# Optimization experiments

Hardware: AMD Instinct MI355X
Metric: run time of the kernel (lower is better)

## Reference

```python
import jax, jax.numpy as jnp
import numpy as np

B, T, C = 2, 2048, 1024
H = 16
HD = C // H  # 64
BLOCK_SIZE = 2048
ROPE_BASE = 10000.0
NEG_INF = float('-inf')


def setup_inputs() -> dict:
    key = jax.random.key(0)
    k1, k2, k3, k4, k5, k6, k7 = jax.random.split(key, 7)
    x = jax.random.normal(k1, (B, T, C), dtype=jnp.float32)
    cumulative_scores = jax.random.normal(k2, (B, T), dtype=jnp.float32)
    padding_mask = jnp.ones((B, BLOCK_SIZE), dtype=jnp.bool_)
    token_index = jax.random.randint(k3, (B, T), 0, BLOCK_SIZE, dtype=jnp.int32)
    c_attn_weight = 0.02 * jax.random.normal(k4, (C, 3 * C), dtype=jnp.float32)
    c_attn_bias = jnp.zeros((3 * C,), dtype=jnp.float32)
    c_proj_weight = 0.02 * jax.random.normal(k5, (C, C), dtype=jnp.float32)
    c_proj_bias = jnp.zeros((C,), dtype=jnp.float32)
    return {
        'x': x,
        'cumulative_scores': cumulative_scores,
        'padding_mask': padding_mask,
        'token_index': token_index,
        'c_attn_weight': c_attn_weight,
        'c_attn_bias': c_attn_bias,
        'c_proj_weight': c_proj_weight,
        'c_proj_bias': c_proj_bias,
    }


def _rotate_half(x):
    x1, x2 = x[..., : x.shape[-1] // 2], x[..., x.shape[-1] // 2:]
    return jnp.concatenate((-x2, x1), axis=-1)


def _forward(x, cumulative_scores, c_attn_weight, c_attn_bias, c_proj_weight,
             c_proj_bias, token_index, padding_mask):
    # qkv projection
    qkv = x @ c_attn_weight + c_attn_bias
    q, k, v = jnp.split(qkv, 3, axis=2)
    q = q.reshape(B, T, H, HD).transpose(0, 2, 1, 3)  # [B,H,T,HD]
    k = k.reshape(B, T, H, HD).transpose(0, 2, 1, 3)
    v = v.reshape(B, T, H, HD).transpose(0, 2, 1, 3)

    # data-dependent per-token rotation amounts (faithful to source: the
    # scatter x.at[..., idx].add(1) with 2D idx accumulates over all batches)
    token_counts = jnp.zeros((B, BLOCK_SIZE), dtype=token_index.dtype)
    token_counts = token_counts.at[..., token_index].add(1)
    inv_counts = 1.0 / (token_counts + 1e-10)  # [B, BLOCK_SIZE] float32
    partial_rotations = jnp.cumsum(
        jnp.take_along_axis(inv_counts, token_index, axis=-1), axis=-1)  # [B,T]

    # RoPE with per-token t
    inv_freq = 1.0 / ROPE_BASE ** (jnp.arange(0, HD, 2, dtype=jnp.float32) / HD)
    freqs = jnp.einsum('bt,j->btj', partial_rotations, inv_freq)  # [B,T,HD/2]
    emb = jnp.concatenate((freqs, freqs), axis=-1)  # [B,T,HD]
    cos = jnp.cos(emb)[:, None, :, :]  # [B,1,T,HD]
    sin = jnp.sin(emb)[:, None, :, :]
    q = q * cos + _rotate_half(q) * sin
    k = k * cos + _rotate_half(k) * sin

    # fork plan: overwrite last channel of q with ones, of k with cum scores
    q = q.at[:, :, :, -1].set(1.0)
    k = k.at[:, :, :, -1].set(jnp.broadcast_to(cumulative_scores[:, None, :], (B, H, T)))

    # causal + padding additive mask
    causal = jnp.where(jnp.tril(jnp.ones((T, T), dtype=jnp.bool_)), 0.0, NEG_INF)  # [T,T]
    pm = jnp.take_along_axis(padding_mask, token_index, axis=1).astype(jnp.float32)  # [B,T]
    pm_outer = pm[:, :, None] * pm[:, None, :]  # [B,T,T]
    pm_add = jnp.where(pm_outer.astype(jnp.bool_), 0.0, NEG_INF)
    mask = causal[None, :, :] + pm_add  # [B,T,T]

    # v scaled by exp(cumulative_scores) along L
    v = v * jnp.exp(cumulative_scores)[:, None, :, None]

    scale = 1.0 / jnp.sqrt(jnp.asarray(HD, dtype=jnp.float32))
    attn = jnp.einsum('bnqd,bnkd->bnqk', q, k) * scale + mask[:, None, :, :]
    attn = jax.nn.softmax(attn, axis=-1)
    y = jnp.einsum('bnqk,bnkd->bnqd', attn, v)
    y = y.transpose(0, 2, 1, 3).reshape(B, T, C)
    return y @ c_proj_weight + c_proj_bias


def reference(x, cumulative_scores, padding_mask, token_index, c_attn_weight,
              c_attn_bias, c_proj_weight, c_proj_bias):
    return _forward(x, cumulative_scores, c_attn_weight, c_attn_bias,
                    c_proj_weight, c_proj_bias, token_index, padding_mask)
```

## Files before the change

kernel.cpp:

```cpp
#include <hip/hip_runtime.h>
#include <hip/hip_bf16.h>
#include <math.h>

#define Bb 2
#define Tt 2048
#define Cc 1024
#define Hh 16
#define HDd 64
#define QSCALE 0.18033688011112042f

typedef __attribute__((ext_vector_type(8))) short short8;
typedef __attribute__((ext_vector_type(4))) short short4v;
typedef __attribute__((ext_vector_type(4))) float f32x4;

#if defined(__has_builtin)
#if __has_builtin(__builtin_amdgcn_global_load_lds)
#define USE_GLL 1
#endif
#endif
#define AS_GLOBAL __attribute__((address_space(1)))
#define AS_LDS    __attribute__((address_space(3)))

__device__ __forceinline__ float bf2f(unsigned short u){
  union { unsigned int i; float f; } v; v.i = ((unsigned int)u)<<16; return v.f;
}
__device__ __forceinline__ unsigned short f2bf(float f){
  union { float f; unsigned int i; } v; v.f = f;
  unsigned int x = v.i;
  return (unsigned short)((x + 0x7fffu + ((x>>16)&1u)) >> 16);
}
__device__ __forceinline__ unsigned int cvtpk_bf16(float lo, float hi){
  unsigned int r;
  asm("v_cvt_pk_bf16_f32 %0, %1, %2" : "=v"(r) : "v"(lo), "v"(hi));
  return r;
}
__device__ __forceinline__ float exp2fast(float x){
  float r; asm("v_exp_f32 %0, %1" : "=v"(r) : "v"(x)); return r;
}
__device__ __forceinline__ f32x4 mfma16(short4v a, short4v b, f32x4 c){
#if defined(__has_builtin)
#if __has_builtin(__builtin_amdgcn_mfma_f32_16x16x16_bf16)
  return __builtin_amdgcn_mfma_f32_16x16x16_bf16(a, b, c, 0, 0, 0);
#elif __has_builtin(__builtin_amdgcn_mfma_f32_16x16x16bf16_1k)
  return __builtin_amdgcn_mfma_f32_16x16x16bf16_1k(a, b, c, 0, 0, 0);
#else
  asm("v_mfma_f32_16x16x16_bf16 %0, %1, %2, %3" : "=v"(c) : "v"(a), "v"(b), "0"(c));
  return c;
#endif
#else
  asm("v_mfma_f32_16x16x16_bf16 %0, %1, %2, %3" : "=v"(c) : "v"(a), "v"(b), "0"(c));
  return c;
#endif
}

__global__ __launch_bounds__(256) void k_f2b(const float* __restrict__ in,
                                             unsigned short* __restrict__ out, int n){
  int i = (blockIdx.x*256 + threadIdx.x)*8;
  if (i >= n) return;
  float4 v0 = *(const float4*)(in + i);
  float4 v1 = *(const float4*)(in + i + 4);
  union { unsigned int u[4]; int4 v; } pk;
  pk.u[0] = cvtpk_bf16(v0.x, v0.y);
  pk.u[1] = cvtpk_bf16(v0.z, v0.w);
  pk.u[2] = cvtpk_bf16(v1.x, v1.y);
  pk.u[3] = cvtpk_bf16(v1.z, v1.w);
  *(int4*)(out + i) = pk.v;
}

__global__ __launch_bounds__(256) void k_transpose_f2b(const float* __restrict__ in,
                                                       unsigned short* __restrict__ out,
                                                       int K, int N){
  __shared__ float tile[32][33];
  int kb = blockIdx.y*32, nb = blockIdx.x*32;
  int tx = threadIdx.x, ty = threadIdx.y;
  #pragma unroll
  for (int i=0;i<4;i++)
    tile[ty+i*8][tx] = in[(size_t)(kb+ty+i*8)*N + nb + tx];
  __syncthreads();
  #pragma unroll
  for (int i=0;i<4;i++)
    out[(size_t)(nb+ty+i*8)*K + kb + tx] = f2bf(tile[tx][ty+i*8]);
}

__global__ __launch_bounds__(1024) void k_scan(const int* __restrict__ tok,
                                               float* __restrict__ cs_t){
  __shared__ int cnt[2048];
  __shared__ float vals[2048];
  __shared__ float psum[1024];
  int b = blockIdx.x;
  int tid = threadIdx.x;
  cnt[tid] = 0; cnt[tid+1024] = 0;
  __syncthreads();
  for (int i = tid; i < Bb*Tt; i += 1024) atomicAdd(&cnt[tok[i]], 1);
  __syncthreads();
  for (int i = tid; i < Tt; i += 1024){
    int idx = tok[b*Tt + i];
    vals[i] = 1.0f / ((float)cnt[idx] + 1e-10f);
  }
  __syncthreads();
  float s0 = vals[2*tid], s1 = vals[2*tid+1];
  psum[tid] = s0 + s1;
  __syncthreads();
  for (int off=1; off<1024; off<<=1){
    float add = (tid>=off) ? psum[tid-off] : 0.0f;
    __syncthreads();
    psum[tid] += add;
    __syncthreads();
  }
  float base = (tid>0) ? psum[tid-1] : 0.0f;
  vals[2*tid]   = base + s0;
  vals[2*tid+1] = base + s0 + s1;
  __syncthreads();
  for (int i = tid; i < Tt*32; i += 1024){
    int t = i >> 5, j = i & 31;
    float invf = exp2f(-(float)j * 0.4152410118609203f);
    float ang = vals[t] * invf;
    float2 cs = make_float2(cosf(ang), sinf(ang));
    *(float2*)&cs_t[((size_t)b*Tt + t)*64 + 2*j] = cs;
  }
}

__global__ __launch_bounds__(256, 4) void k_gemmQKV(const unsigned short* __restrict__ A,
                                                    const unsigned short* __restrict__ Bt,
                                                    const float* __restrict__ bias,
                                                    const float* __restrict__ cs_t,
                                                    const float* __restrict__ cum,
                                                    unsigned short* __restrict__ Qo,
                                                    unsigned short* __restrict__ Ko,
                                                    unsigned short* __restrict__ VTo){
  __shared__ union {
    unsigned short ab[2][128][32];
    unsigned short vb[32][140];
  } sm;
  const int K = 1024, N = 3072;
  int mb = blockIdx.y*128, nb = blockIdx.x*128;
  int tid = threadIdx.x;
  int wave = tid>>6, lane = tid&63;
  int wr = wave>>1, wc = wave&1;
  int lrow = lane&15, lhi = lane>>4;
  f32x4 acc[4][4] = {};
  int r0 = tid>>2;
  int gd = tid&3;
  int gs0 = (gd ^ ((r0>>1)&3)) << 3;
  const unsigned short* Arow0 = A  + (size_t)(mb + r0)*K      + gs0;
  const unsigned short* Arow1 = A  + (size_t)(mb + r0 + 64)*K + gs0;
  const unsigned short* Brow0 = Bt + (size_t)(nb + r0)*K      + gs0;
  const unsigned short* Brow1 = Bt + (size_t)(nb + r0 + 64)*K + gs0;
#ifdef USE_GLL
  for (int kb=0; kb<K; kb+=32){
    __builtin_amdgcn_global_load_lds((const AS_GLOBAL void*)(Arow0 + kb),
                                     (AS_LDS void*)&sm.ab[0][r0][gd*8],    16, 0, 0);
    __builtin_amdgcn_global_load_lds((const AS_GLOBAL void*)(Arow1 + kb),
                                     (AS_LDS void*)&sm.ab[0][r0+64][gd*8], 16, 0, 0);
    __builtin_amdgcn_global_load_lds((const AS_GLOBAL void*)(Brow0 + kb),
                                     (AS_LDS void*)&sm.ab[1][r0][gd*8],    16, 0, 0);
    __builtin_amdgcn_global_load_lds((const AS_GLOBAL void*)(Brow1 + kb),
                                     (AS_LDS void*)&sm.ab[1][r0+64][gd*8], 16, 0, 0);
    __syncthreads();
    short8 af[4], bf[4];
    #pragma unroll
    for (int m=0;m<4;m++){
      int R = 64*wr + 16*m + lrow;
      af[m] = *(const short8*)&sm.ab[0][R][(lhi^((R>>1)&3))<<3];
    }
    #pragma unroll
    for (int n=0;n<4;n++){
      int R = 64*wc + 16*n + lrow;
      bf[n] = *(const short8*)&sm.ab[1][R][(lhi^((R>>1)&3))<<3];
    }
    #pragma unroll
    for (int m=0;m<4;m++)
      #pragma unroll
      for (int n=0;n<4;n++)
        acc[m][n] = __builtin_amdgcn_mfma_f32_16x16x32_bf16(af[m], bf[n], acc[m][n], 0,0,0);
    __syncthreads();
  }
#else
  for (int kb=0; kb<K; kb+=32){
    int4 a0 = *(const int4*)(Arow0 + kb);
    int4 a1 = *(const int4*)(Arow1 + kb);
    int4 b0 = *(const int4*)(Brow0 + kb);
    int4 b1 = *(const int4*)(Brow1 + kb);
    __syncthreads();
    *(int4*)&sm.ab[0][r0][gd*8]    = a0;
    *(int4*)&sm.ab[0][r0+64][gd*8] = a1;
    *(int4*)&sm.ab[1][r0][gd*8]    = b0;
    *(int4*)&sm.ab[1][r0+64][gd*8] = b1;
    __syncthreads();
    short8 af[4], bf[4];
    #pragma unroll
    for (int m=0;m<4;m++){
      int R = 64*wr + 16*m + lrow;
      af[m] = *(const short8*)&sm.ab[0][R][(lhi^((R>>1)&3))<<3];
    }
    #pragma unroll
    for (int n=0;n<4;n++){
      int R = 64*wc + 16*n + lrow;
      bf[n] = *(const short8*)&sm.ab[1][R][(lhi^((R>>1)&3))<<3];
    }
    #pragma unroll
    for (int m=0;m<4;m++)
      #pragma unroll
      for (int n=0;n<4;n++)
        acc[m][n] = __builtin_amdgcn_mfma_f32_16x16x32_bf16(af[m], bf[n], acc[m][n], 0,0,0);
  }
#endif
  int type = nb >> 10;
  int h0 = (nb >> 6) & 15;
  int h  = h0 + wc;
  int b_ = mb >> 11;
  int tb_ = mb & 2047;
  float bz[4];
  #pragma unroll
  for (int n=0;n<4;n++) bz[n] = bias[nb + 64*wc + 16*n + lrow];

  if (type < 2){
    unsigned short* dst = (type==0) ? Qo : Ko;
    #pragma unroll
    for (int m=0;m<4;m++)
      #pragma unroll
      for (int q=0;q<4;q++){
        int rl = 64*wr + 16*m + 4*lhi + q;
        int row = mb + rl;
        float2 cs0 = *(const float2*)&cs_t[(size_t)row*64 + 2*lrow];
        float2 cs1 = *(const float2*)&cs_t[(size_t)row*64 + 32 + 2*lrow];
        float a0 = acc[m][0][q] + bz[0];
        float a1 = acc[m][1][q] + bz[1];
        float a2 = acc[m][2][q] + bz[2];
        float a3 = acc[m][3][q] + bz[3];
        float r0v = a0*cs0.x - a2*cs0.y;
        float r1v = a1*cs1.x - a3*cs1.y;
        float r2v = a2*cs0.x + a0*cs0.y;
        float r3v = a3*cs1.x + a1*cs1.y;
        if (type==0){
          if (lrow==15) r3v = 1.0f;
          r0v *= QSCALE; r1v *= QSCALE; r2v *= QSCALE; r3v *= QSCALE;
        } else {
          if (lrow==15) r3v = cum[row];
        }
        size_t base = (((size_t)b_*Hh + h)*Tt + (row & 2047))*HDd + lrow;
        dst[base]      = f2bf(r0v);
        dst[base + 16] = f2bf(r1v);
        dst[base + 32] = f2bf(r2v);
        dst[base + 48] = f2bf(r3v);
      }
  } else {
    for (int pass=0; pass<4; pass++){
      __syncthreads();
      if (wr == (pass>>1)){
        int m0 = 2*(pass&1);
        #pragma unroll
        for (int mm=0; mm<2; mm++){
          int m = m0 + mm;
          #pragma unroll
          for (int q=0;q<4;q++){
            int rl32 = 16*mm + 4*lhi + q;
            float vs = __expf(cum[mb + 32*pass + rl32]);
            sm.vb[rl32][64*wc + lrow]      = f2bf((acc[m][0][q]+bz[0])*vs);
            sm.vb[rl32][64*wc + 16+lrow]   = f2bf((acc[m][1][q]+bz[1])*vs);
            sm.vb[rl32][64*wc + 32+lrow]   = f2bf((acc[m][2][q]+bz[2])*vs);
            sm.vb[rl32][64*wc + 48+lrow]   = f2bf((acc[m][3][q]+bz[3])*vs);
          }
        }
      }
      __syncthreads();
      #pragma unroll
      for (int i=0;i<16;i++){
        int idx = i*256 + tid;
        int t_l = idx & 31;
        int dh  = idx >> 5;
        int d   = dh & 63;
        int hh  = dh >> 6;
        VTo[(((size_t)b_*Hh + h0 + hh)*HDd + d)*Tt + tb_ + 32*pass + t_l] = sm.vb[t_l][64*hh + d];
      }
    }
  }
}

__global__ __launch_bounds__(256) void k_gemm64(const unsigned short* __restrict__ A,
                                                const unsigned short* __restrict__ Bt,
                                                const float* __restrict__ bias,
                                                float* __restrict__ Cout,
                                                int M, int N, int K){
  __shared__ unsigned short As[64][32];
  __shared__ unsigned short Bs[128][32];
  int mb = blockIdx.y*64, nb = blockIdx.x*128;
  int tid = threadIdx.x;
  int wave = tid>>6, lane = tid&63;
  int wr = wave>>1, wc = wave&1;
  int lrow = lane&15, lhi = lane>>4;
  f32x4 acc[2][4] = {};
  int r0 = tid>>2;
  int gd = tid&3;
  int gs0 = (gd ^ ((r0>>1)&3)) << 3;
  const unsigned short* Arow  = A  + (size_t)(mb + r0)*K      + gs0;
  const unsigned short* Brow0 = Bt + (size_t)(nb + r0)*K      + gs0;
  const unsigned short* Brow1 = Bt + (size_t)(nb + r0 + 64)*K + gs0;
#ifdef USE_GLL
  for (int kb=0; kb<K; kb+=32){
    __builtin_amdgcn_global_load_lds((const AS_GLOBAL void*)(Arow + kb),
                                     (AS_LDS void*)&As[r0][gd*8],    16, 0, 0);
    __builtin_amdgcn_global_load_lds((const AS_GLOBAL void*)(Brow0 + kb),
                                     (AS_LDS void*)&Bs[r0][gd*8],    16, 0, 0);
    __builtin_amdgcn_global_load_lds((const AS_GLOBAL void*)(Brow1 + kb),
                                     (AS_LDS void*)&Bs[r0+64][gd*8], 16, 0, 0);
    __syncthreads();
    short8 af[2], bf[4];
    #pragma unroll
    for (int m=0;m<2;m++){
      int R = 32*wr + 16*m + lrow;
      af[m] = *(const short8*)&As[R][(lhi^((R>>1)&3))<<3];
    }
    #pragma unroll
    for (int n=0;n<4;n++){
      int R = 64*wc + 16*n + lrow;
      bf[n] = *(const short8*)&Bs[R][(lhi^((R>>1)&3))<<3];
    }
    #pragma unroll
    for (int m=0;m<2;m++)
      #pragma unroll
      for (int n=0;n<4;n++)
        acc[m][n] = __builtin_amdgcn_mfma_f32_16x16x32_bf16(af[m], bf[n], acc[m][n], 0,0,0);
    __syncthreads();
  }
#else
  for (int kb=0; kb<K; kb+=32){
    int4 a0 = *(const int4*)(Arow + kb);
    int4 b0 = *(const int4*)(Brow0 + kb);
    int4 b1 = *(const int4*)(Brow1 + kb);
    __syncthreads();
    *(int4*)&As[r0][gd*8]    = a0;
    *(int4*)&Bs[r0][gd*8]    = b0;
    *(int4*)&Bs[r0+64][gd*8] = b1;
    __syncthreads();
    short8 af[2], bf[4];
    #pragma unroll
    for (int m=0;m<2;m++){
      int R = 32*wr + 16*m + lrow;
      af[m] = *(const short8*)&As[R][(lhi^((R>>1)&3))<<3];
    }
    #pragma unroll
    for (int n=0;n<4;n++){
      int R = 64*wc + 16*n + lrow;
      bf[n] = *(const short8*)&Bs[R][(lhi^((R>>1)&3))<<3];
    }
    #pragma unroll
    for (int m=0;m<2;m++)
      #pragma unroll
      for (int n=0;n<4;n++)
        acc[m][n] = __builtin_amdgcn_mfma_f32_16x16x32_bf16(af[m], bf[n], acc[m][n], 0,0,0);
  }
#endif
  #pragma unroll
  for (int m=0;m<2;m++)
    #pragma unroll
    for (int n=0;n<4;n++)
      #pragma unroll
      for (int q=0;q<4;q++){
        int row = mb + 32*wr + 16*m + 4*lhi + q;
        int col = nb + 64*wc + 16*n + lrow;
        Cout[(size_t)row*N + col] = acc[m][n][q] + bias[col];
      }
}

__global__ __launch_bounds__(512, 4) void k_attn8(const unsigned short* __restrict__ Q,
                                                  const unsigned short* __restrict__ K,
                                                  const unsigned short* __restrict__ VT,
                                                  unsigned short* __restrict__ Y){
  __shared__ __align__(16) char smem[65536];
  typedef unsigned short (*tile_t)[2][4096];
  tile_t Ks = (tile_t)smem;
  tile_t Vs = (tile_t)(smem + 32768);
  float (*cmb)[64][35] = (float (*)[64][35])smem;

  int bh = blockIdx.y; int b = bh >> 4, h = bh & 15;
  int s_ = blockIdx.x;
  int tid = threadIdx.x;
  int wave = tid>>6, lane = tid&63;
  int wpair = wave & 3, p = wave >> 2;
  int lrow = lane&15, lhi = lane>>4;
  const unsigned short* Qh = Q + (((size_t)b*Hh + h)*Tt)*HDd;
  const unsigned short* Kh = K + (((size_t)b*Hh + h)*Tt)*HDd;
  const unsigned short* Vh = VT + (((size_t)b*Hh + h)*HDd)*Tt;
  int qL0 = 64*s_ + 16*wpair;
  int qH0 = 1984 - 64*s_ + 16*wpair;
  short8 qfL0 = *(const short8*)&Qh[(size_t)(qL0+lrow)*HDd + 8*lhi];
  short8 qfL1 = *(const short8*)&Qh[(size_t)(qL0+lrow)*HDd + 32 + 8*lhi];
  short8 qfH0 = *(const short8*)&Qh[(size_t)(qH0+lrow)*HDd + 8*lhi];
  short8 qfH1 = *(const short8*)&Qh[(size_t)(qH0+lrow)*HDd + 32 + 8*lhi];
  f32x4 oL[4] = {}, oH[4] = {};
  float lsL = 0.0f, lsH = 0.0f;
  int rowL = qL0 + lrow, rowH = qH0 + lrow;
  int ntL = s_ + 1;
  int NTH = 32 - s_;
  int NI  = (NTH + 1) >> 1;

  int kr = tid >> 3, kc = tid & 7;
  int o_ = tid * 16;
  int ksrc = kr*HDd + ((kc ^ (kr&7)) << 3);
  int vsrc = kr*Tt  + ((kc ^ (kr&7)) << 3);

#ifdef USE_GLL
#define STAGE2(bufi, base_) do { \
    __builtin_amdgcn_global_load_lds((const AS_GLOBAL void*)(Kh + (size_t)(base_)*64*HDd + ksrc), \
        (AS_LDS void*)((AS_LDS char*)&Ks[bufi][0][0] + o_), 16, 0, 0); \
    __builtin_amdgcn_global_load_lds((const AS_GLOBAL void*)(Vh + (size_t)(base_)*64 + vsrc), \
        (AS_LDS void*)((AS_LDS char*)&Vs[bufi][0][0] + o_), 16, 0, 0); \
    if ((base_)+1 < NTH){ \
      __builtin_amdgcn_global_load_lds((const AS_GLOBAL void*)(Kh + (size_t)((base_)+1)*64*HDd + ksrc), \
          (AS_LDS void*)((AS_LDS char*)&Ks[bufi][1][0] + o_), 16, 0, 0); \
      __builtin_amdgcn_global_load_lds((const AS_GLOBAL void*)(Vh + (size_t)((base_)+1)*64 + vsrc), \
          (AS_LDS void*)((AS_LDS char*)&Vs[bufi][1][0] + o_), 16, 0, 0); \
    } \
  } while(0)
#else
#define STAGE2(bufi, base_) do { \
    int4 a_ = *(const int4*)(Kh + (size_t)(base_)*64*HDd + ksrc); \
    int4 c_ = *(const int4*)(Vh + (size_t)(base_)*64 + vsrc); \
    *(int4*)((char*)&Ks[bufi][0][0] + o_) = a_; \
    *(int4*)((char*)&Vs[bufi][0][0] + o_) = c_; \
    if ((base_)+1 < NTH){ \
      int4 b_ = *(const int4*)(Kh + (size_t)((base_)+1)*64*HDd + ksrc); \
      int4 d_ = *(const int4*)(Vh + (size_t)((base_)+1)*64 + vsrc); \
      *(int4*)((char*)&Ks[bufi][1][0] + o_) = b_; \
      *(int4*)((char*)&Vs[bufi][1][0] + o_) = d_; \
    } \
  } while(0)
#endif

  STAGE2(0, 0);
  int buf = 0;
  for (int i = 0; i < NI; i++){
    __syncthreads();
    if (i+1 < NI) STAGE2(buf^1, 2*(i+1));
    int kt = 2*i + p;
    if (kt < NTH){
      int k0 = kt*64;
      bool doL = (kt < ntL);
      const unsigned short* Kbase = &Ks[buf][p][0];
      const unsigned short* Vbase = &Vs[buf][p][0];
      f32x4 sL[4] = {}, sH[4] = {};
      __builtin_amdgcn_s_setprio(1);
      #pragma unroll
      for (int j=0;j<4;j++){
        int krow = 16*j + lrow;
        #pragma unroll
        for (int ks=0;ks<2;ks++){
          int dgrp = (4*ks + lhi) ^ (krow&7);
          short8 kf = *(const short8*)&Kbase[krow*64 + dgrp*8];
          sH[j] = __builtin_amdgcn_mfma_f32_16x16x32_bf16(kf, ks ? qfH1 : qfH0, sH[j], 0,0,0);
          if (doL) sL[j] = __builtin_amdgcn_mfma_f32_16x16x32_bf16(kf, ks ? qfL1 : qfL0, sL[j], 0,0,0);
        }
      }
      __builtin_amdgcn_s_setprio(0);
      short4v paH[4], paL[4];
      {
        bool diagH = (k0 + 63 >= qH0);
        #pragma unroll
        for (int j=0;j<4;j++){
          int kbase = k0 + 16*j + 4*lhi;
          float p0 = exp2fast(sH[j][0]);
          float p1 = exp2fast(sH[j][1]);
          float p2 = exp2fast(sH[j][2]);
          float p3 = exp2fast(sH[j][3]);
          if (diagH){
            if (kbase + 0 > rowH) p0 = 0.0f;
            if (kbase + 1 > rowH) p1 = 0.0f;
            if (kbase + 2 > rowH) p2 = 0.0f;
            if (kbase + 3 > rowH) p3 = 0.0f;
          }
          lsH += (p0 + p1) + (p2 + p3);
          union { unsigned int u[2]; short4v v; } pk;
          pk.u[0] = cvtpk_bf16(p0, p1);
          pk.u[1] = cvtpk_bf16(p2, p3);
          paH[j] = pk.v;
        }
      }
      if (doL){
        bool diagL = (k0 + 63 >= qL0);
        #pragma unroll
        for (int j=0;j<4;j++){
          int kbase = k0 + 16*j + 4*lhi;
          float p0 = exp2fast(sL[j][0]);
          float p1 = exp2fast(sL[j][1]);
          float p2 = exp2fast(sL[j][2]);
          float p3 = exp2fast(sL[j][3]);
          if (diagL){
            if (kbase + 0 > rowL) p0 = 0.0f;
            if (kbase + 1 > rowL) p1 = 0.0f;
            if (kbase + 2 > rowL) p2 = 0.0f;
            if (kbase + 3 > rowL) p3 = 0.0f;
          }
          lsL += (p0 + p1) + (p2 + p3);
          union { unsigned int u[2]; short4v v; } pk;
          pk.u[0] = cvtpk_bf16(p0, p1);
          pk.u[1] = cvtpk_bf16(p2, p3);
          paL[j] = pk.v;
        }
      }
      __builtin_amdgcn_s_setprio(1);
      #pragma unroll
      for (int jp=0;jp<4;jp++){
        int vrow = 16*jp + lrow;
        #pragma unroll
        for (int j=0;j<4;j++){
          int byte_in_row = ((((2*j + (lhi>>1)) ^ (vrow&7)) << 4) | ((lhi&1) << 3));
          short4v vf = *(const short4v*)((const char*)&Vbase[vrow*64] + byte_in_row);
          oH[jp] = mfma16(vf, paH[j], oH[jp]);
          if (doL) oL[jp] = mfma16(vf, paL[j], oL[jp]);
        }
      }
      __builtin_amdgcn_s_setprio(0);
    }
    buf ^= 1;
  }

  __syncthreads();
  if (p == 1){
    float* c = &cmb[wpair][lane][0];
    #pragma unroll
    for (int jp=0;jp<4;jp++)
      #pragma unroll
      for (int r=0;r<4;r++){
        c[4*jp+r]    = oL[jp][r];
        c[16+4*jp+r] = oH[jp][r];
      }
    c[32] = lsL; c[33] = lsH;
  }
  __syncthreads();
  if (p == 0){
    const float* c = &cmb[wpair][lane][0];
    #pragma unroll
    for (int jp=0;jp<4;jp++)
      #pragma unroll
      for (int r=0;r<4;r++){
        oL[jp][r] += c[4*jp+r];
        oH[jp][r] += c[16+4*jp+r];
      }
    lsL += c[32]; lsH += c[33];
    lsL += __shfl_xor(lsL, 16); lsL += __shfl_xor(lsL, 32);
    lsH += __shfl_xor(lsH, 16); lsH += __shfl_xor(lsH, 32);
    float invL = 1.0f / lsL, invH = 1.0f / lsH;
    size_t rbL = ((size_t)b*Tt + qL0 + lrow)*Cc + h*HDd + 4*lhi;
    size_t rbH = ((size_t)b*Tt + qH0 + lrow)*Cc + h*HDd + 4*lhi;
    #pragma unroll
    for (int jp=0;jp<4;jp++){
      unsigned int l0 = cvtpk_bf16(oL[jp][0]*invL, oL[jp][1]*invL);
      unsigned int l1 = cvtpk_bf16(oL[jp][2]*invL, oL[jp][3]*invL);
      unsigned int h0_ = cvtpk_bf16(oH[jp][0]*invH, oH[jp][1]*invH);
      unsigned int h1_ = cvtpk_bf16(oH[jp][2]*invH, oH[jp][3]*invH);
      *(unsigned long long*)&Y[rbL + 16*jp] = (unsigned long long)l0 | ((unsigned long long)l1<<32);
      *(unsigned long long*)&Y[rbH + 16*jp] = (unsigned long long)h0_ | ((unsigned long long)h1_<<32);
    }
  }
#undef STAGE2
}

extern "C" void kernel_launch(void* const* d_in, const int* in_sizes, int n_in,
                              void* d_out, int out_size, void* d_ws, size_t ws_size,
                              hipStream_t stream){
  const float* x     = (const float*)d_in[0];
  const float* cum   = (const float*)d_in[1];
  const int*   tok   = (const int*)d_in[3];
  const float* Wqkv  = (const float*)d_in[4];
  const float* bqkv  = (const float*)d_in[5];
  const float* Wproj = (const float*)d_in[6];
  const float* bproj = (const float*)d_in[7];

  char* ws = (char*)d_ws;
  size_t off = 0;
  auto alloc = [&](size_t bytes)->void*{
    void* p = ws + off; off += (bytes + 255) & ~(size_t)255; return p;
  };
  unsigned short* wqkvT = (unsigned short*)alloc((size_t)3072*1024*2);
  unsigned short* wprojT= (unsigned short*)alloc((size_t)1024*1024*2);
  unsigned short* xb    = (unsigned short*)alloc((size_t)4096*1024*2);
  unsigned short* Qb    = (unsigned short*)alloc((size_t)Bb*Hh*Tt*HDd*2);
  unsigned short* Kb    = (unsigned short*)alloc((size_t)Bb*Hh*Tt*HDd*2);
  unsigned short* VTb   = (unsigned short*)alloc((size_t)Bb*Hh*Tt*HDd*2);
  float* cs_t           = (float*)alloc((size_t)Bb*Tt*64*4);
  unsigned short* Y     = xb;

  k_f2b<<<dim3(4096*1024/8/256), dim3(256), 0, stream>>>(x, xb, 4096*1024);
  k_transpose_f2b<<<dim3(3072/32, 1024/32), dim3(32,8), 0, stream>>>(Wqkv, wqkvT, 1024, 3072);
  k_transpose_f2b<<<dim3(1024/32, 1024/32), dim3(32,8), 0, stream>>>(Wproj, wprojT, 1024, 1024);
  k_scan<<<dim3(Bb), dim3(1024), 0, stream>>>(tok, cs_t);
  k_gemmQKV<<<dim3(3072/128, 4096/128), dim3(256), 0, stream>>>(xb, wqkvT, bqkv, cs_t, cum, Qb, Kb, VTb);
  k_attn8<<<dim3(16, Bb*Hh), dim3(512), 0, stream>>>(Qb, Kb, VTb, Y);
  k_gemm64<<<dim3(1024/128, 4096/64), dim3(256), 0, stream>>>(Y, wprojT, bproj, (float*)d_out, 4096, 1024, 1024);
}
```

Measured before the change: 140.2 us.

## Widen QKV GEMM K-step to 64 and single-buffer attention LDS for occupancy

The QKV GEMM now stages a 64-wide K slice per iteration with an 8-way XOR swizzle. That halves the number of barrier pairs and issues two MFMA sub-steps per load. The attention kernel drops its double-buffered K/V LDS tiles in favour of a single buffer (36 KB instead of 64 KB) and raises launch bounds to 8 blocks per SM to get more resident waves. The cost is that loads are no longer prefetched behind compute in attention, and an extra barrier is added per iteration.

```diff
diff --git a/kernel.cpp b/kernel.cpp
--- a/kernel.cpp
+++ b/kernel.cpp
@@ -129,7 +129,7 @@
                                                     unsigned short* __restrict__ Ko,
                                                     unsigned short* __restrict__ VTo){
   __shared__ union {
-    unsigned short ab[2][128][32];
+    unsigned short ab[2][128][64];
     unsigned short vb[32][140];
   } sm;
   const int K = 1024, N = 3072;
@@ -139,70 +139,78 @@
   int wr = wave>>1, wc = wave&1;
   int lrow = lane&15, lhi = lane>>4;
   f32x4 acc[4][4] = {};
-  int r0 = tid>>2;
-  int gd = tid&3;
-  int gs0 = (gd ^ ((r0>>1)&3)) << 3;
-  const unsigned short* Arow0 = A  + (size_t)(mb + r0)*K      + gs0;
-  const unsigned short* Arow1 = A  + (size_t)(mb + r0 + 64)*K + gs0;
-  const unsigned short* Brow0 = Bt + (size_t)(nb + r0)*K      + gs0;
-  const unsigned short* Brow1 = Bt + (size_t)(nb + r0 + 64)*K + gs0;
+  int r0 = tid>>3;
+  int g0 = tid&7;
+  int gsw = (g0 ^ (r0&7)) << 3;
+  const unsigned short* Asrc = A  + (size_t)(mb + r0)*K + gsw;
+  const unsigned short* Bsrc = Bt + (size_t)(nb + r0)*K + gsw;
+  const size_t rstep = (size_t)32*K;
 #ifdef USE_GLL
-  for (int kb=0; kb<K; kb+=32){
-    __builtin_amdgcn_global_load_lds((const AS_GLOBAL void*)(Arow0 + kb),
-                                     (AS_LDS void*)&sm.ab[0][r0][gd*8],    16, 0, 0);
-    __builtin_amdgcn_global_load_lds((const AS_GLOBAL void*)(Arow1 + kb),
-                                     (AS_LDS void*)&sm.ab[0][r0+64][gd*8], 16, 0, 0);
-    __builtin_amdgcn_global_load_lds((const AS_GLOBAL void*)(Brow0 + kb),
-                                     (AS_LDS void*)&sm.ab[1][r0][gd*8],    16, 0, 0);
-    __builtin_amdgcn_global_load_lds((const AS_GLOBAL void*)(Brow1 + kb),
-                                     (AS_LDS void*)&sm.ab[1][r0+64][gd*8], 16, 0, 0);
-    __syncthreads();
-    short8 af[4], bf[4];
-    #pragma unroll
-    for (int m=0;m<4;m++){
-      int R = 64*wr + 16*m + lrow;
-      af[m] = *(const short8*)&sm.ab[0][R][(lhi^((R>>1)&3))<<3];
-    }
-    #pragma unroll
-    for (int n=0;n<4;n++){
-      int R = 64*wc + 16*n + lrow;
-      bf[n] = *(const short8*)&sm.ab[1][R][(lhi^((R>>1)&3))<<3];
-    }
-    #pragma unroll
-    for (int m=0;m<4;m++)
-      #pragma unroll
-      for (int n=0;n<4;n++)
-        acc[m][n] = __builtin_amdgcn_mfma_f32_16x16x32_bf16(af[m], bf[n], acc[m][n], 0,0,0);
+  for (int kb=0; kb<K; kb+=64){
+    #pragma unroll
+    for (int i=0;i<4;i++){
+      __builtin_amdgcn_global_load_lds((const AS_GLOBAL void*)(Asrc + i*rstep + kb),
+                                       (AS_LDS void*)&sm.ab[0][r0+32*i][g0*8], 16, 0, 0);
+      __builtin_amdgcn_global_load_lds((const AS_GLOBAL void*)(Bsrc + i*rstep + kb),
+                                       (AS_LDS void*)&sm.ab[1][r0+32*i][g0*8], 16, 0, 0);
+    }
+    __syncthreads();
+    #pragma unroll
+    for (int ks=0; ks<2; ks++){
+      short8 af[4], bf[4];
+      #pragma unroll
+      for (int m=0;m<4;m++){
+        int R = 64*wr + 16*m + lrow;
+        af[m] = *(const short8*)&sm.ab[0][R][((4*ks+lhi)^(R&7))<<3];
+      }
+      #pragma unroll
+      for (int n=0;n<4;n++){
+        int R = 64*wc + 16*n + lrow;
+        bf[n] = *(const short8*)&sm.ab[1][R][((4*ks+lhi)^(R&7))<<3];
+      }
+      #pragma unroll
+      for (int m=0;m<4;m++)
+        #pragma unroll
+        for (int n=0;n<4;n++)
+          acc[m][n] = __builtin_amdgcn_mfma_f32_16x16x32_bf16(af[m], bf[n], acc[m][n], 0,0,0);
+    }
     __syncthreads();
   }
 #else
-  for (int kb=0; kb<K; kb+=32){
-    int4 a0 = *(const int4*)(Arow0 + kb);
-    int4 a1 = *(const int4*)(Arow1 + kb);
-    int4 b0 = *(const int4*)(Brow0 + kb);
-    int4 b1 = *(const int4*)(Brow1 + kb);
-    __syncthreads();
-    *(int4*)&sm.ab[0][r0][gd*8]    = a0;
-    *(int4*)&sm.ab[0][r0+64][gd*8] = a1;
-    *(int4*)&sm.ab[1][r0][gd*8]    = b0;
-    *(int4*)&sm.ab[1][r0+64][gd*8] = b1;
-    __syncthreads();
-    short8 af[4], bf[4];
-    #pragma unroll
-    for (int m=0;m<4;m++){
-      int R = 64*wr + 16*m + lrow;
-      af[m] = *(const short8*)&sm.ab[0][R][(lhi^((R>>1)&3))<<3];
-    }
-    #pragma unroll
-    for (int n=0;n<4;n++){
-      int R = 64*wc + 16*n + lrow;
-      bf[n] = *(const short8*)&sm.ab[1][R][(lhi^((R>>1)&3))<<3];
-    }
-    #pragma unroll
-    for (int m=0;m<4;m++)
-      #pragma unroll
-      for (int n=0;n<4;n++)
-        acc[m][n] = __builtin_amdgcn_mfma_f32_16x16x32_bf16(af[m], bf[n], acc[m][n], 0,0,0);
+  for (int kb=0; kb<K; kb+=64){
+    int4 st[8];
+    #pragma unroll
+    for (int i=0;i<4;i++){
+      st[2*i]   = *(const int4*)(Asrc + i*rstep + kb);
+      st[2*i+1] = *(const int4*)(Bsrc + i*rstep + kb);
+    }
+    __syncthreads();
+    #pragma unroll
+    for (int i=0;i<4;i++){
+      *(int4*)&sm.ab[0][r0+32*i][g0*8] = st[2*i];
+      *(int4*)&sm.ab[1][r0+32*i][g0*8] = st[2*i+1];
+    }
+    __syncthreads();
+    #pragma unroll
+    for (int ks=0; ks<2; ks++){
+      short8 af[4], bf[4];
+      #pragma unroll
+      for (int m=0;m<4;m++){
+        int R = 64*wr + 16*m + lrow;
+        af[m] = *(const short8*)&sm.ab[0][R][((4*ks+lhi)^(R&7))<<3];
+      }
+      #pragma unroll
+      for (int n=0;n<4;n++){
+        int R = 64*wc + 16*n + lrow;
+        bf[n] = *(const short8*)&sm.ab[1][R][((4*ks+lhi)^(R&7))<<3];
+      }
+      #pragma unroll
+      for (int m=0;m<4;m++)
+        #pragma unroll
+        for (int n=0;n<4;n++)
+          acc[m][n] = __builtin_amdgcn_mfma_f32_16x16x32_bf16(af[m], bf[n], acc[m][n], 0,0,0);
+    }
+    __syncthreads();
   }
 #endif
   int type = nb >> 10;
@@ -363,14 +371,13 @@
       }
 }
 
-__global__ __launch_bounds__(512, 4) void k_attn8(const unsigned short* __restrict__ Q,
-                                                  const unsigned short* __restrict__ K,
-                                                  const unsigned short* __restrict__ VT,
-                                                  unsigned short* __restrict__ Y){
-  __shared__ __align__(16) char smem[65536];
-  typedef unsigned short (*tile_t)[2][4096];
-  tile_t Ks = (tile_t)smem;
-  tile_t Vs = (tile_t)(smem + 32768);
+__global__ __launch_bounds__(512, 8) void k_attn10(const unsigned short* __restrict__ Q,
+                                                   const unsigned short* __restrict__ K,
+                                                   const unsigned short* __restrict__ VT,
+                                                   unsigned short* __restrict__ Y){
+  __shared__ __align__(16) char smem[36864];
+  unsigned short (*Ks)[4096] = (unsigned short (*)[4096])smem;
+  unsigned short (*Vs)[4096] = (unsigned short (*)[4096])(smem + 16384);
   float (*cmb)[64][35] = (float (*)[64][35])smem;
 
   int bh = blockIdx.y; int b = bh >> 4, h = bh & 15;
@@ -401,44 +408,43 @@
   int vsrc = kr*Tt  + ((kc ^ (kr&7)) << 3);
 
 #ifdef USE_GLL
-#define STAGE2(bufi, base_) do { \
+#define STAGE2(base_) do { \
     __builtin_amdgcn_global_load_lds((const AS_GLOBAL void*)(Kh + (size_t)(base_)*64*HDd + ksrc), \
-        (AS_LDS void*)((AS_LDS char*)&Ks[bufi][0][0] + o_), 16, 0, 0); \
+        (AS_LDS void*)((AS_LDS char*)&Ks[0][0] + o_), 16, 0, 0); \
     __builtin_amdgcn_global_load_lds((const AS_GLOBAL void*)(Vh + (size_t)(base_)*64 + vsrc), \
-        (AS_LDS void*)((AS_LDS char*)&Vs[bufi][0][0] + o_), 16, 0, 0); \
+        (AS_LDS void*)((AS_LDS char*)&Vs[0][0] + o_), 16, 0, 0); \
     if ((base_)+1 < NTH){ \
       __builtin_amdgcn_global_load_lds((const AS_GLOBAL void*)(Kh + (size_t)((base_)+1)*64*HDd + ksrc), \
-          (AS_LDS void*)((AS_LDS char*)&Ks[bufi][1][0] + o_), 16, 0, 0); \
+          (AS_LDS void*)((AS_LDS char*)&Ks[1][0] + o_), 16, 0, 0); \
       __builtin_amdgcn_global_load_lds((const AS_GLOBAL void*)(Vh + (size_t)((base_)+1)*64 + vsrc), \
-          (AS_LDS void*)((AS_LDS char*)&Vs[bufi][1][0] + o_), 16, 0, 0); \
+          (AS_LDS void*)((AS_LDS char*)&Vs[1][0] + o_), 16, 0, 0); \
     } \
   } while(0)
 #else
-#define STAGE2(bufi, base_) do { \
+#define STAGE2(base_) do { \
     int4 a_ = *(const int4*)(Kh + (size_t)(base_)*64*HDd + ksrc); \
     int4 c_ = *(const int4*)(Vh + (size_t)(base_)*64 + vsrc); \
-    *(int4*)((char*)&Ks[bufi][0][0] + o_) = a_; \
-    *(int4*)((char*)&Vs[bufi][0][0] + o_) = c_; \
+    *(int4*)((char*)&Ks[0][0] + o_) = a_; \
+    *(int4*)((char*)&Vs[0][0] + o_) = c_; \
     if ((base_)+1 < NTH){ \
       int4 b_ = *(const int4*)(Kh + (size_t)((base_)+1)*64*HDd + ksrc); \
       int4 d_ = *(const int4*)(Vh + (size_t)((base_)+1)*64 + vsrc); \
-      *(int4*)((char*)&Ks[bufi][1][0] + o_) = b_; \
-      *(int4*)((char*)&Vs[bufi][1][0] + o_) = d_; \
+      *(int4*)&((char*)&Ks[1][0])[o_] = b_; \
+      *(int4*)&((char*)&Vs[1][0])[o_] = d_; \
     } \
   } while(0)
 #endif
 
-  STAGE2(0, 0);
-  int buf = 0;
   for (int i = 0; i < NI; i++){
     __syncthreads();
-    if (i+1 < NI) STAGE2(buf^1, 2*(i+1));
+    STAGE2(2*i);
+    __syncthreads();
     int kt = 2*i + p;
     if (kt < NTH){
       int k0 = kt*64;
       bool doL = (kt < ntL);
-      const unsigned short* Kbase = &Ks[buf][p][0];
-      const unsigned short* Vbase = &Vs[buf][p][0];
+      const unsigned short* Kbase = &Ks[p][0];
+      const unsigned short* Vbase = &Vs[p][0];
       f32x4 sL[4] = {}, sH[4] = {};
       __builtin_amdgcn_s_setprio(1);
       #pragma unroll
@@ -512,7 +518,6 @@
       }
       __builtin_amdgcn_s_setprio(0);
     }
-    buf ^= 1;
   }
 
   __syncthreads();
@@ -586,6 +591,6 @@
   k_transpose_f2b<<<dim3(1024/32, 1024/32), dim3(32,8), 0, stream>>>(Wproj, wprojT, 1024, 1024);
   k_scan<<<dim3(Bb), dim3(1024), 0, stream>>>(tok, cs_t);
   k_gemmQKV<<<dim3(3072/128, 4096/128), dim3(256), 0, stream>>>(xb, wqkvT, bqkv, cs_t, cum, Qb, Kb, VTb);
-  k_attn8<<<dim3(16, Bb*Hh), dim3(512), 0, stream>>>(Qb, Kb, VTb, Y);
+  k_attn10<<<dim3(16, Bb*Hh), dim3(512), 0, stream>>>(Qb, Kb, VTb, Y);
   k_gemm64<<<dim3(1024/128, 4096/64), dim3(256), 0, stream>>>(Y, wprojT, bproj, (float*)d_out, 4096, 1024, 1024);
 }
```

Result: slower. 352.7 us (+151.6%).

## Double-buffer QKV GEMM LDS staging and merge weight transpose launches

Applied to the files above, without the earlier changes.

The QKV GEMM now keeps two LDS stage buffers. It issues the next k-tile's global-to-LDS loads before computing on the current tile, cutting one barrier per iteration and raising MFMA priority with s_setprio. The two weight transpose-convert kernels are merged into one launch that picks its matrix by blockIdx.z, with early exit for out-of-range blocks. The trade-off is double the LDS per block for the staging buffers, which may lower occupancy. The vb union member is still reused after the loop, so a final barrier was added.

```diff
diff --git a/kernel.cpp b/kernel.cpp
--- a/kernel.cpp
+++ b/kernel.cpp
@@ -67,10 +67,17 @@
   *(int4*)(out + i) = pk.v;
 }
 
-__global__ __launch_bounds__(256) void k_transpose_f2b(const float* __restrict__ in,
-                                                       unsigned short* __restrict__ out,
-                                                       int K, int N){
+__global__ __launch_bounds__(256) void k_transpose_f2b(const float* __restrict__ w0,
+                                                       const float* __restrict__ w1,
+                                                       unsigned short* __restrict__ o0,
+                                                       unsigned short* __restrict__ o1){
   __shared__ float tile[32][33];
+  const int K = 1024;
+  int which = blockIdx.z;
+  const float* in = which ? w1 : w0;
+  unsigned short* out = which ? o1 : o0;
+  int N = which ? 1024 : 3072;
+  if (blockIdx.x*32 >= N) return;
   int kb = blockIdx.y*32, nb = blockIdx.x*32;
   int tx = threadIdx.x, ty = threadIdx.y;
   #pragma unroll
@@ -129,7 +136,7 @@
                                                     unsigned short* __restrict__ Ko,
                                                     unsigned short* __restrict__ VTo){
   __shared__ union {
-    unsigned short ab[2][128][32];
+    unsigned short ab[2][2][128][32];
     unsigned short vb[32][140];
   } sm;
   const int K = 1024, N = 3072;
@@ -147,64 +154,55 @@
   const unsigned short* Brow0 = Bt + (size_t)(nb + r0)*K      + gs0;
   const unsigned short* Brow1 = Bt + (size_t)(nb + r0 + 64)*K + gs0;
 #ifdef USE_GLL
+#define QSTAGE(bufi, kb_) do { \
+    __builtin_amdgcn_global_load_lds((const AS_GLOBAL void*)(Arow0 + (kb_)), \
+        (AS_LDS void*)&sm.ab[bufi][0][r0][gd*8],    16, 0, 0); \
+    __builtin_amdgcn_global_load_lds((const AS_GLOBAL void*)(Arow1 + (kb_)), \
+        (AS_LDS void*)&sm.ab[bufi][0][r0+64][gd*8], 16, 0, 0); \
+    __builtin_amdgcn_global_load_lds((const AS_GLOBAL void*)(Brow0 + (kb_)), \
+        (AS_LDS void*)&sm.ab[bufi][1][r0][gd*8],    16, 0, 0); \
+    __builtin_amdgcn_global_load_lds((const AS_GLOBAL void*)(Brow1 + (kb_)), \
+        (AS_LDS void*)&sm.ab[bufi][1][r0+64][gd*8], 16, 0, 0); \
+  } while(0)
+#else
+#define QSTAGE(bufi, kb_) do { \
+    int4 a0_ = *(const int4*)(Arow0 + (kb_)); \
+    int4 a1_ = *(const int4*)(Arow1 + (kb_)); \
+    int4 b0_ = *(const int4*)(Brow0 + (kb_)); \
+    int4 b1_ = *(const int4*)(Brow1 + (kb_)); \
+    *(int4*)&sm.ab[bufi][0][r0][gd*8]    = a0_; \
+    *(int4*)&sm.ab[bufi][0][r0+64][gd*8] = a1_; \
+    *(int4*)&sm.ab[bufi][1][r0][gd*8]    = b0_; \
+    *(int4*)&sm.ab[bufi][1][r0+64][gd*8] = b1_; \
+  } while(0)
+#endif
+  QSTAGE(0, 0);
+  int buf = 0;
   for (int kb=0; kb<K; kb+=32){
-    __builtin_amdgcn_global_load_lds((const AS_GLOBAL void*)(Arow0 + kb),
-                                     (AS_LDS void*)&sm.ab[0][r0][gd*8],    16, 0, 0);
-    __builtin_amdgcn_global_load_lds((const AS_GLOBAL void*)(Arow1 + kb),
-                                     (AS_LDS void*)&sm.ab[0][r0+64][gd*8], 16, 0, 0);
-    __builtin_amdgcn_global_load_lds((const AS_GLOBAL void*)(Brow0 + kb),
-                                     (AS_LDS void*)&sm.ab[1][r0][gd*8],    16, 0, 0);
-    __builtin_amdgcn_global_load_lds((const AS_GLOBAL void*)(Brow1 + kb),
-                                     (AS_LDS void*)&sm.ab[1][r0+64][gd*8], 16, 0, 0);
-    __syncthreads();
+    __syncthreads();
+    if (kb+32 < K) QSTAGE(buf^1, kb+32);
     short8 af[4], bf[4];
     #pragma unroll
     for (int m=0;m<4;m++){
       int R = 64*wr + 16*m + lrow;
-      af[m] = *(const short8*)&sm.ab[0][R][(lhi^((R>>1)&3))<<3];
+      af[m] = *(const short8*)&sm.ab[buf][0][R][(lhi^((R>>1)&3))<<3];
     }
     #pragma unroll
     for (int n=0;n<4;n++){
       int R = 64*wc + 16*n + lrow;
-      bf[n] = *(const short8*)&sm.ab[1][R][(lhi^((R>>1)&3))<<3];
-    }
+      bf[n] = *(const short8*)&sm.ab[buf][1][R][(lhi^((R>>1)&3))<<3];
+    }
+    __builtin_amdgcn_s_setprio(1);
     #pragma unroll
     for (int m=0;m<4;m++)
       #pragma unroll
       for (int n=0;n<4;n++)
         acc[m][n] = __builtin_amdgcn_mfma_f32_16x16x32_bf16(af[m], bf[n], acc[m][n], 0,0,0);
-    __syncthreads();
-  }
-#else
-  for (int kb=0; kb<K; kb+=32){
-    int4 a0 = *(const int4*)(Arow0 + kb);
-    int4 a1 = *(const int4*)(Arow1 + kb);
-    int4 b0 = *(const int4*)(Brow0 + kb);
-    int4 b1 = *(const int4*)(Brow1 + kb);
-    __syncthreads();
-    *(int4*)&sm.ab[0][r0][gd*8]    = a0;
-    *(int4*)&sm.ab[0][r0+64][gd*8] = a1;
-    *(int4*)&sm.ab[1][r0][gd*8]    = b0;
-    *(int4*)&sm.ab[1][r0+64][gd*8] = b1;
-    __syncthreads();
-    short8 af[4], bf[4];
-    #pragma unroll
-    for (int m=0;m<4;m++){
-      int R = 64*wr + 16*m + lrow;
-      af[m] = *(const short8*)&sm.ab[0][R][(lhi^((R>>1)&3))<<3];
-    }
-    #pragma unroll
-    for (int n=0;n<4;n++){
-      int R = 64*wc + 16*n + lrow;
-      bf[n] = *(const short8*)&sm.ab[1][R][(lhi^((R>>1)&3))<<3];
-    }
-    #pragma unroll
-    for (int m=0;m<4;m++)
-      #pragma unroll
-      for (int n=0;n<4;n++)
-        acc[m][n] = __builtin_amdgcn_mfma_f32_16x16x32_bf16(af[m], bf[n], acc[m][n], 0,0,0);
-  }
-#endif
+    __builtin_amdgcn_s_setprio(0);
+    buf ^= 1;
+  }
+#undef QSTAGE
+  __syncthreads();
   int type = nb >> 10;
   int h0 = (nb >> 6) & 15;
   int h  = h0 + wc;
@@ -582,8 +580,7 @@
   unsigned short* Y     = xb;
 
   k_f2b<<<dim3(4096*1024/8/256), dim3(256), 0, stream>>>(x, xb, 4096*1024);
-  k_transpose_f2b<<<dim3(3072/32, 1024/32), dim3(32,8), 0, stream>>>(Wqkv, wqkvT, 1024, 3072);
-  k_transpose_f2b<<<dim3(1024/32, 1024/32), dim3(32,8), 0, stream>>>(Wproj, wprojT, 1024, 1024);
+  k_transpose_f2b<<<dim3(3072/32, 1024/32, 2), dim3(32,8), 0, stream>>>(Wqkv, Wproj, wqkvT, wprojT);
   k_scan<<<dim3(Bb), dim3(1024), 0, stream>>>(tok, cs_t);
   k_gemmQKV<<<dim3(3072/128, 4096/128), dim3(256), 0, stream>>>(xb, wqkvT, bqkv, cs_t, cum, Qb, Kb, VTb);
   k_attn8<<<dim3(16, Bb*Hh), dim3(512), 0, stream>>>(Qb, Kb, VTb, Y);
```

After: 136.6 us. 2.6% less time.
